# Optimization experiments

Hardware: AMD Instinct MI355X
Metric: run time of the kernel (lower is better)

## Reference

```python
import jax, jax.numpy as jnp
import numpy as np

INPUT_SIZE, HIDDEN, LEVELS = 64, 256, 2
T, B = 2048, 128


def _lstm_layer(x_seq, h0, c0, W_ih, W_hh, b_ih, b_hh):
    """Run one LSTM layer over the full sequence. x_seq: [T,B,D] -> hs: [T,B,H].
    PyTorch gate order: i, f, g, o."""
    def step(carry, x_t):
        h, c = carry
        z = x_t @ W_ih.T + b_ih + h @ W_hh.T + b_hh  # [B, 4H]
        i, f, g, o = jnp.split(z, 4, axis=-1)
        i = jax.nn.sigmoid(i)
        f = jax.nn.sigmoid(f)
        g = jnp.tanh(g)
        o = jax.nn.sigmoid(o)
        c = f * c + i * g
        h = o * jnp.tanh(c)
        return (h, c), h
    _, hs = jax.lax.scan(step, (h0, c0), x_seq)
    return hs


def setup_inputs() -> dict:
    key = jax.random.key(0)
    ks = jax.random.split(key, 16)
    s = 1.0 / np.sqrt(HIDDEN)
    inp = {
        "x": jax.random.normal(ks[0], (T, B, INPUT_SIZE), dtype=jnp.float32),
        "h0": jax.random.uniform(ks[1], (LEVELS, B, HIDDEN), dtype=jnp.float32),
        "c0": jax.random.uniform(ks[2], (LEVELS, B, HIDDEN), dtype=jnp.float32),
        # layer 0 (input -> hidden)
        "W_ih0": jax.random.uniform(ks[3], (4 * HIDDEN, INPUT_SIZE), jnp.float32, -s, s),
        "W_hh0": jax.random.uniform(ks[4], (4 * HIDDEN, HIDDEN), jnp.float32, -s, s),
        "b_ih0": jax.random.uniform(ks[5], (4 * HIDDEN,), jnp.float32, -s, s),
        "b_hh0": jax.random.uniform(ks[6], (4 * HIDDEN,), jnp.float32, -s, s),
        # layer 1 (hidden -> hidden)
        "W_ih1": jax.random.uniform(ks[7], (4 * HIDDEN, HIDDEN), jnp.float32, -s, s),
        "W_hh1": jax.random.uniform(ks[8], (4 * HIDDEN, HIDDEN), jnp.float32, -s, s),
        "b_ih1": jax.random.uniform(ks[9], (4 * HIDDEN,), jnp.float32, -s, s),
        "b_hh1": jax.random.uniform(ks[10], (4 * HIDDEN,), jnp.float32, -s, s),
        # linear head hidden -> 1
        "W_lin": jax.random.uniform(ks[11], (1, HIDDEN), jnp.float32, -s, s),
        "b_lin": jax.random.uniform(ks[12], (1,), jnp.float32, -s, s),
    }
    return inp


def reference(x, h0, c0, W_ih0, W_hh0, b_ih0, b_hh0, W_ih1, W_hh1, b_ih1, b_hh1, W_lin, b_lin):
    hs0 = _lstm_layer(x, h0[0], c0[0], W_ih0, W_hh0, b_ih0, b_hh0)   # [T,B,H]
    hs1 = _lstm_layer(hs0, h0[1], c0[1], W_ih1, W_hh1, b_ih1, b_hh1)  # [T,B,H]
    out = hs1 @ W_lin.T + b_lin  # [T,B,1]
    return out[..., 0]  # [T,B] (matches torch stack().squeeze())
```

## Files before the change

### kernel.cpp

```cpp
#include <hip/hip_runtime.h>

constexpr int TT   = 2048;
constexpr int NB   = 128;
constexpr int NI   = 64;
constexpr int NH   = 256;
constexpr int NGRP = 128;
constexpr int NWG  = 256;
constexpr int NTHR = 512;
constexpr int R0   = 8;
constexpr int R1   = 16;
constexpr int HLAG = 8;
constexpr int SLOT = (NH / 2) * NB;

__device__ __align__(256) unsigned g_p0[128];
__device__ __align__(256) unsigned g_p1[128];
__device__ unsigned g_cnt = 0, g_gen = 0;

__device__ __forceinline__ float sigm(float v) { return 1.0f / (1.0f + __expf(-v)); }
__device__ __forceinline__ float tanhfast(float v) {
    float e = __expf(2.0f * v);
    return 1.0f - 2.0f / (e + 1.0f);
}
__device__ __forceinline__ float asfl(unsigned u) { return __uint_as_float(u); }
__device__ __forceinline__ unsigned f2bf(float f) {
    unsigned u = __float_as_uint(f);
    return (u + 0x7fffu + ((u >> 16) & 1u)) >> 16;
}

__device__ __forceinline__ unsigned long long ldq(const unsigned* p) {
    return __hip_atomic_load((const unsigned long long*)p, __ATOMIC_RELAXED,
                             __HIP_MEMORY_SCOPE_AGENT);
}
__device__ __forceinline__ unsigned ldd(const unsigned* p) {
    return __hip_atomic_load(p, __ATOMIC_RELAXED, __HIP_MEMORY_SCOPE_AGENT);
}
__device__ __forceinline__ void std_(unsigned* p, unsigned v) {
    __hip_atomic_store(p, v, __ATOMIC_RELAXED, __HIP_MEMORY_SCOPE_AGENT);
}

__device__ __forceinline__ void pollall(unsigned n0, unsigned n1, int lane) {
    const unsigned* p0 = &g_p0[lane << 1];
    const unsigned* p1 = &g_p1[lane << 1];
    for (;;) {
        unsigned long long a = ldq(p0);
        unsigned long long b = ldq(p1);
        bool ok = ((unsigned)a >= n0) && ((unsigned)(a >> 32) >= n0) &&
                  ((unsigned)b >= n1) && ((unsigned)(b >> 32) >= n1);
        if (__all(ok)) return;
        __builtin_amdgcn_s_sleep(1);
    }
}

__device__ __forceinline__ void gridbar(unsigned k, bool last) {
    __syncthreads();
    if (threadIdx.x == 0) {
        __threadfence();
        unsigned a = __hip_atomic_fetch_add(&g_cnt, 1u, __ATOMIC_ACQ_REL,
                                            __HIP_MEMORY_SCOPE_AGENT);
        if (a == k * NWG - 1u) {
            if (last) {
                __hip_atomic_store(&g_cnt, 0u, __ATOMIC_RELAXED, __HIP_MEMORY_SCOPE_AGENT);
                __hip_atomic_store(&g_gen, 0u, __ATOMIC_RELEASE, __HIP_MEMORY_SCOPE_AGENT);
            } else {
                __hip_atomic_store(&g_gen, k, __ATOMIC_RELEASE, __HIP_MEMORY_SCOPE_AGENT);
            }
        } else if (!last) {
            while (__hip_atomic_load(&g_gen, __ATOMIC_RELAXED,
                                     __HIP_MEMORY_SCOPE_AGENT) < k)
                __builtin_amdgcn_s_sleep(1);
        }
        __threadfence();
    }
    __syncthreads();
}

#define STEPQ(Q, HA, HB)                                   \
    acc[0]  += w00.Q * (HA); acc[1]  += w00.Q * (HB);      \
    acc[2]  += w01.Q * (HA); acc[3]  += w01.Q * (HB);      \
    acc[4]  += w02.Q * (HA); acc[5]  += w02.Q * (HB);      \
    acc[6]  += w03.Q * (HA); acc[7]  += w03.Q * (HB);      \
    acc[8]  += w10.Q * (HA); acc[9]  += w10.Q * (HB);      \
    acc[10] += w11.Q * (HA); acc[11] += w11.Q * (HB);      \
    acc[12] += w12.Q * (HA); acc[13] += w12.Q * (HB);      \
    acc[14] += w13.Q * (HA); acc[15] += w13.Q * (HB);

#define LOADW(W, K, kk)                                                        \
    float4 w00 = *(const float4*)((W) + (size_t)(0 * NH + j0    ) * (K) + (kk)); \
    float4 w01 = *(const float4*)((W) + (size_t)(1 * NH + j0    ) * (K) + (kk)); \
    float4 w02 = *(const float4*)((W) + (size_t)(2 * NH + j0    ) * (K) + (kk)); \
    float4 w03 = *(const float4*)((W) + (size_t)(3 * NH + j0    ) * (K) + (kk)); \
    float4 w10 = *(const float4*)((W) + (size_t)(0 * NH + j0 + 1) * (K) + (kk)); \
    float4 w11 = *(const float4*)((W) + (size_t)(1 * NH + j0 + 1) * (K) + (kk)); \
    float4 w12 = *(const float4*)((W) + (size_t)(2 * NH + j0 + 1) * (K) + (kk)); \
    float4 w13 = *(const float4*)((W) + (size_t)(3 * NH + j0 + 1) * (K) + (kk));

__device__ __forceinline__ void partH_bf(const float* __restrict__ W, int j0,
                                         int kbase,
                                         const unsigned* __restrict__ hd,
                                         int lane, float* acc) {
    const unsigned* hp = hd + (size_t)(kbase >> 1) * NB + (lane << 1);
    #pragma unroll 4
    for (int i = 0; i < 16; ++i) {
        const int kk = kbase + (i << 2);
        LOADW(W, NH, kk)
        unsigned long long q0 = ldq(hp + (size_t)(2 * i) * NB);
        unsigned long long q1 = ldq(hp + (size_t)(2 * i + 1) * NB);
        unsigned d00 = (unsigned)q0, d01 = (unsigned)(q0 >> 32);
        unsigned d10 = (unsigned)q1, d11 = (unsigned)(q1 >> 32);
        STEPQ(x, asfl(d00 << 16),          asfl(d01 << 16))
        STEPQ(y, asfl(d00 & 0xffff0000u),  asfl(d01 & 0xffff0000u))
        STEPQ(z, asfl(d10 << 16),          asfl(d11 << 16))
        STEPQ(w, asfl(d10 & 0xffff0000u),  asfl(d11 & 0xffff0000u))
    }
}

__device__ __forceinline__ void partX(const float* __restrict__ W, int j0,
                                      int k0, const float* __restrict__ xp,
                                      int lane, float* acc) {
    #pragma unroll
    for (int i4 = 0; i4 < 4; ++i4) {
        const int kk = k0 + (i4 << 2);
        LOADW(W, NI, kk)
        float4 xa = *(const float4*)(xp + (size_t)(lane << 1) * NI + kk);
        float4 xb = *(const float4*)(xp + (size_t)((lane << 1) + 1) * NI + kk);
        STEPQ(x, xa.x, xb.x)
        STEPQ(y, xa.y, xb.y)
        STEPQ(z, xa.z, xb.z)
        STEPQ(w, xa.w, xb.w)
    }
}

__global__ void __launch_bounds__(NTHR, 2) lstm2(
    const float* __restrict__ x,
    const float* __restrict__ h0in, const float* __restrict__ c0in,
    const float* __restrict__ Wih0, const float* __restrict__ Whh0,
    const float* __restrict__ bih0, const float* __restrict__ bhh0,
    const float* __restrict__ Wih1, const float* __restrict__ Whh1,
    const float* __restrict__ bih1, const float* __restrict__ bhh1,
    const float* __restrict__ Wlin, const float* __restrict__ blin,
    float* __restrict__ out,
    unsigned* __restrict__ h0d, unsigned* __restrict__ h1d)
{
    __shared__ __align__(16) float4 zp4[16 * NB];
    __shared__ float red[4];
    __shared__ unsigned go_w;

    const int tid  = threadIdx.x;
    const int gid  = blockIdx.x;
    const bool is1 = gid >= NGRP;
    const int g    = is1 ? gid - NGRP : gid;
    const int j0   = g * 2;
    const int lane = tid & 63;
    const int wv   = __builtin_amdgcn_readfirstlane(tid >> 6);

    unsigned* ownp = is1 ? g_p1 : g_p0;

    float4 bsA = make_float4(0, 0, 0, 0), bsB = bsA;
    float cA = 0.f, cB = 0.f;
    if (tid < 128) {
        const float* bi = is1 ? bih1 : bih0;
        const float* bh = is1 ? bhh1 : bhh0;
        bsA.x = bi[0 * NH + j0] + bh[0 * NH + j0];
        bsA.y = bi[1 * NH + j0] + bh[1 * NH + j0];
        bsA.z = bi[2 * NH + j0] + bh[2 * NH + j0];
        bsA.w = bi[3 * NH + j0] + bh[3 * NH + j0];
        bsB.x = bi[0 * NH + j0 + 1] + bh[0 * NH + j0 + 1];
        bsB.y = bi[1 * NH + j0 + 1] + bh[1 * NH + j0 + 1];
        bsB.z = bi[2 * NH + j0 + 1] + bh[2 * NH + j0 + 1];
        bsB.w = bi[3 * NH + j0 + 1] + bh[3 * NH + j0 + 1];
        const float* cbase = c0in + (is1 ? 1 : 0) * NB * NH + (size_t)tid * NH + j0;
        cA = cbase[0]; cB = cbase[1];
        const float* hbase = h0in + (is1 ? 1 : 0) * NB * NH + (size_t)tid * NH + j0;
        unsigned d = (f2bf(hbase[1]) << 16) | f2bf(hbase[0]);
        unsigned* hT = is1 ? h1d : h0d;
        const int islot = is1 ? (R1 - 1) : (R0 - 1);
        std_(hT + (size_t)islot * SLOT + (size_t)g * NB + tid, d);
    }
    if (tid == 0) go_w = 0;
    const float blv = blin[0];
    asm volatile("s_waitcnt vmcnt(0)" ::: "memory");
    __syncthreads();
    if (tid == 0) std_(&ownp[g], 1u);

    if (!is1) {
        for (int s = 0; s < TT + HLAG; ++s) {
            const unsigned tgt = (unsigned)(s + 1);
            unsigned need0 = (s < TT) ? (unsigned)(s + 1) : 0u;
            unsigned need1 = (s >= R0) ? (unsigned)(s - R0 + 2) : 0u;
            if (wv == 0) {
                pollall(need0, need1, lane);
                if (lane == 0)
                    __hip_atomic_store(&go_w, tgt, __ATOMIC_RELAXED,
                                       __HIP_MEMORY_SCOPE_WORKGROUP);
            } else {
                while (__hip_atomic_load(&go_w, __ATOMIC_RELAXED,
                                         __HIP_MEMORY_SCOPE_WORKGROUP) < tgt) {}
            }

            if (s < TT) {
                float acc[16] = {0,0,0,0,0,0,0,0,0,0,0,0,0,0,0,0};
                if (wv < 4)
                    partH_bf(Whh0, j0, wv * 64,
                             h0d + (size_t)((s + R0 - 1) & (R0 - 1)) * SLOT, lane, acc);
                else
                    partX(Wih0, j0, (wv - 4) * 16, x + (size_t)s * NB * NI, lane, acc);
                const int base0 = ((wv << 1) + 0) * NB + (lane << 1);
                const int base1 = ((wv << 1) + 1) * NB + (lane << 1);
                zp4[base0]     = make_float4(acc[0],  acc[2],  acc[4],  acc[6]);
                zp4[base0 + 1] = make_float4(acc[1],  acc[3],  acc[5],  acc[7]);
                zp4[base1]     = make_float4(acc[8],  acc[10], acc[12], acc[14]);
                zp4[base1 + 1] = make_float4(acc[9],  acc[11], acc[13], acc[15]);
            }
            if (s >= HLAG && tid >= 256) {
                const int u = s - HLAG;
                const int k = tid - 256;
                unsigned d = ldd(h1d + (size_t)(u & (R1 - 1)) * SLOT
                                 + (size_t)(k >> 1) * NB + g);
                float hv = (k & 1) ? asfl(d & 0xffff0000u) : asfl(d << 16);
                float p = Wlin[k] * hv;
                #pragma unroll
                for (int off = 32; off; off >>= 1) p += __shfl_down(p, off);
                if (lane == 0) red[wv - 4] = p;
            }
            __syncthreads();

            if (s < TT && tid < 128) {
                float4 zA = bsA, zB = bsB;
                #pragma unroll
                for (int q = 0; q < 8; ++q) {
                    float4 a = zp4[(q * 2 + 0) * NB + tid];
                    float4 b = zp4[(q * 2 + 1) * NB + tid];
                    zA.x += a.x; zA.y += a.y; zA.z += a.z; zA.w += a.w;
                    zB.x += b.x; zB.y += b.y; zB.z += b.z; zB.w += b.w;
                }
                float iA = sigm(zA.x), fA = sigm(zA.y), gA = tanhfast(zA.z), oA = sigm(zA.w);
                cA = fA * cA + iA * gA;
                float hA = oA * tanhfast(cA);
                float iB = sigm(zB.x), fB = sigm(zB.y), gB = tanhfast(zB.z), oB = sigm(zB.w);
                cB = fB * cB + iB * gB;
                float hB = oB * tanhfast(cB);
                unsigned d = (f2bf(hB) << 16) | f2bf(hA);
                std_(h0d + (size_t)(s & (R0 - 1)) * SLOT + (size_t)g * NB + tid, d);
            }
            if (s >= HLAG && tid == 256)
                out[(size_t)(s - HLAG) * NB + g] = red[0] + red[1] + red[2] + red[3] + blv;

            asm volatile("s_waitcnt vmcnt(0)" ::: "memory");
            __syncthreads();
            if (s < TT && tid == 0) std_(&g_p0[g], (unsigned)(s + 2));
        }
    } else {
        for (int t = 0; t < TT; ++t) {
            const unsigned tgt = (unsigned)(t + 1);
            unsigned need0 = (unsigned)(t + 2);
            unsigned need1 = (unsigned)(t + 1);
            if (wv == 0) {
                pollall(need0, need1, lane);
                if (lane == 0)
                    __hip_atomic_store(&go_w, tgt, __ATOMIC_RELAXED,
                                       __HIP_MEMORY_SCOPE_WORKGROUP);
            } else {
                while (__hip_atomic_load(&go_w, __ATOMIC_RELAXED,
                                         __HIP_MEMORY_SCOPE_WORKGROUP) < tgt) {}
            }

            float acc[16] = {0,0,0,0,0,0,0,0,0,0,0,0,0,0,0,0};
            if (wv < 4)
                partH_bf(Wih1, j0, wv * 64,
                         h0d + (size_t)(t & (R0 - 1)) * SLOT, lane, acc);
            else
                partH_bf(Whh1, j0, (wv - 4) * 64,
                         h1d + (size_t)((t + R1 - 1) & (R1 - 1)) * SLOT, lane, acc);
            const int base0 = ((wv << 1) + 0) * NB + (lane << 1);
            const int base1 = ((wv << 1) + 1) * NB + (lane << 1);
            zp4[base0]     = make_float4(acc[0],  acc[2],  acc[4],  acc[6]);
            zp4[base0 + 1] = make_float4(acc[1],  acc[3],  acc[5],  acc[7]);
            zp4[base1]     = make_float4(acc[8],  acc[10], acc[12], acc[14]);
            zp4[base1 + 1] = make_float4(acc[9],  acc[11], acc[13], acc[15]);
            __syncthreads();

            if (tid < 128) {
                float4 zA = bsA, zB = bsB;
                #pragma unroll
                for (int q = 0; q < 8; ++q) {
                    float4 a = zp4[(q * 2 + 0) * NB + tid];
                    float4 b = zp4[(q * 2 + 1) * NB + tid];
                    zA.x += a.x; zA.y += a.y; zA.z += a.z; zA.w += a.w;
                    zB.x += b.x; zB.y += b.y; zB.z += b.z; zB.w += b.w;
                }
                float iA = sigm(zA.x), fA = sigm(zA.y), gA = tanhfast(zA.z), oA = sigm(zA.w);
                cA = fA * cA + iA * gA;
                float hA = oA * tanhfast(cA);
                float iB = sigm(zB.x), fB = sigm(zB.y), gB = tanhfast(zB.z), oB = sigm(zB.w);
                cB = fB * cB + iB * gB;
                float hB = oB * tanhfast(cB);
                unsigned d = (f2bf(hB) << 16) | f2bf(hA);
                std_(h1d + (size_t)(t & (R1 - 1)) * SLOT + (size_t)g * NB + tid, d);
            }
            asm volatile("s_waitcnt vmcnt(0)" ::: "memory");
            __syncthreads();
            if (tid == 0) std_(&g_p1[g], (unsigned)(t + 2));
        }
    }

    gridbar(1, false);
    if (gid == 0 && tid < 128) {
        std_(&g_p0[tid], 0u);
        std_(&g_p1[tid], 0u);
    }
    asm volatile("s_waitcnt vmcnt(0)" ::: "memory");
    gridbar(2, true);
}

extern "C" void kernel_launch(void* const* d_in, const int* in_sizes, int n_in,
                              void* d_out, int out_size, void* d_ws, size_t ws_size,
                              hipStream_t stream)
{
    const float* x    = (const float*)d_in[0];
    const float* h0in = (const float*)d_in[1];
    const float* c0in = (const float*)d_in[2];
    const float* Wih0 = (const float*)d_in[3];
    const float* Whh0 = (const float*)d_in[4];
    const float* bih0 = (const float*)d_in[5];
    const float* bhh0 = (const float*)d_in[6];
    const float* Wih1 = (const float*)d_in[7];
    const float* Whh1 = (const float*)d_in[8];
    const float* bih1 = (const float*)d_in[9];
    const float* bhh1 = (const float*)d_in[10];
    const float* Wlin = (const float*)d_in[11];
    const float* blin = (const float*)d_in[12];
    float* out = (float*)d_out;

    unsigned* h0d = (unsigned*)d_ws;
    unsigned* h1d = h0d + (size_t)R0 * SLOT;

    void* args[] = { &x, &h0in, &c0in, &Wih0, &Whh0, &bih0, &bhh0,
                     &Wih1, &Whh1, &bih1, &bhh1, &Wlin, &blin,
                     &out, &h0d, &h1d };
    hipLaunchCooperativeKernel((void*)lstm2, dim3(NWG), dim3(NTHR), args, 0, stream);
}
```

Before: 23.03 ms.

## Repartition LSTM work: four hidden units by half batch per workgroup

Each workgroup now owns 4 hidden units across 64 batch columns instead of 2 hidden units across all 128 columns. Each lane handles one batch column against two pairs of weight rows, instead of two columns against one pair. The shared-memory partial-sum layout, the gate reduction indexing and the bf16 h-state write addressing are rewritten to match. The aim is to halve the h-state each workgroup reads from global memory per step. In exchange, per-workgroup weight traffic doubles and each lane loads narrower h values.

```diff
diff --git a/kernel.cpp b/kernel.cpp
--- a/kernel.cpp
+++ b/kernel.cpp
@@ -74,59 +74,64 @@
     __syncthreads();
 }
 
-#define STEPQ(Q, HA, HB)                                   \
-    acc[0]  += w00.Q * (HA); acc[1]  += w00.Q * (HB);      \
-    acc[2]  += w01.Q * (HA); acc[3]  += w01.Q * (HB);      \
-    acc[4]  += w02.Q * (HA); acc[5]  += w02.Q * (HB);      \
-    acc[6]  += w03.Q * (HA); acc[7]  += w03.Q * (HB);      \
-    acc[8]  += w10.Q * (HA); acc[9]  += w10.Q * (HB);      \
-    acc[10] += w11.Q * (HA); acc[11] += w11.Q * (HB);      \
-    acc[12] += w12.Q * (HA); acc[13] += w12.Q * (HB);      \
-    acc[14] += w13.Q * (HA); acc[15] += w13.Q * (HB);
-
-#define LOADW(W, K, kk)                                                        \
-    float4 w00 = *(const float4*)((W) + (size_t)(0 * NH + j0    ) * (K) + (kk)); \
-    float4 w01 = *(const float4*)((W) + (size_t)(1 * NH + j0    ) * (K) + (kk)); \
-    float4 w02 = *(const float4*)((W) + (size_t)(2 * NH + j0    ) * (K) + (kk)); \
-    float4 w03 = *(const float4*)((W) + (size_t)(3 * NH + j0    ) * (K) + (kk)); \
-    float4 w10 = *(const float4*)((W) + (size_t)(0 * NH + j0 + 1) * (K) + (kk)); \
-    float4 w11 = *(const float4*)((W) + (size_t)(1 * NH + j0 + 1) * (K) + (kk)); \
-    float4 w12 = *(const float4*)((W) + (size_t)(2 * NH + j0 + 1) * (K) + (kk)); \
-    float4 w13 = *(const float4*)((W) + (size_t)(3 * NH + j0 + 1) * (K) + (kk));
-
-__device__ __forceinline__ void partH_bf(const float* __restrict__ W, int j0,
-                                         int kbase,
-                                         const unsigned* __restrict__ hd,
-                                         int lane, float* acc) {
-    const unsigned* hp = hd + (size_t)(kbase >> 1) * NB + (lane << 1);
+#define LOADWJ(W, K, kk, jj)                                                       \
+    float4 w00 = *(const float4*)((W) + (size_t)(0 * NH + (jj)    ) * (K) + (kk)); \
+    float4 w01 = *(const float4*)((W) + (size_t)(1 * NH + (jj)    ) * (K) + (kk)); \
+    float4 w02 = *(const float4*)((W) + (size_t)(2 * NH + (jj)    ) * (K) + (kk)); \
+    float4 w03 = *(const float4*)((W) + (size_t)(3 * NH + (jj)    ) * (K) + (kk)); \
+    float4 w10 = *(const float4*)((W) + (size_t)(0 * NH + (jj) + 1) * (K) + (kk)); \
+    float4 w11 = *(const float4*)((W) + (size_t)(1 * NH + (jj) + 1) * (K) + (kk)); \
+    float4 w12 = *(const float4*)((W) + (size_t)(2 * NH + (jj) + 1) * (K) + (kk)); \
+    float4 w13 = *(const float4*)((W) + (size_t)(3 * NH + (jj) + 1) * (K) + (kk));
+
+#define STEP1(Q, H, A)                                     \
+    (A)[0] += w00.Q * (H); (A)[1] += w01.Q * (H);          \
+    (A)[2] += w02.Q * (H); (A)[3] += w03.Q * (H);          \
+    (A)[4] += w10.Q * (H); (A)[5] += w11.Q * (H);          \
+    (A)[6] += w12.Q * (H); (A)[7] += w13.Q * (H);
+
+__device__ __forceinline__ void partH4(const float* __restrict__ W, int j0,
+                                       int kbase,
+                                       const unsigned* __restrict__ hd,
+                                       int col, float* acc) {
+    const unsigned* hp = hd + (size_t)(kbase >> 1) * NB + col;
     #pragma unroll 4
     for (int i = 0; i < 16; ++i) {
         const int kk = kbase + (i << 2);
-        LOADW(W, NH, kk)
-        unsigned long long q0 = ldq(hp + (size_t)(2 * i) * NB);
-        unsigned long long q1 = ldq(hp + (size_t)(2 * i + 1) * NB);
-        unsigned d00 = (unsigned)q0, d01 = (unsigned)(q0 >> 32);
-        unsigned d10 = (unsigned)q1, d11 = (unsigned)(q1 >> 32);
-        STEPQ(x, asfl(d00 << 16),          asfl(d01 << 16))
-        STEPQ(y, asfl(d00 & 0xffff0000u),  asfl(d01 & 0xffff0000u))
-        STEPQ(z, asfl(d10 << 16),          asfl(d11 << 16))
-        STEPQ(w, asfl(d10 & 0xffff0000u),  asfl(d11 & 0xffff0000u))
-    }
-}
-
-__device__ __forceinline__ void partX(const float* __restrict__ W, int j0,
-                                      int k0, const float* __restrict__ xp,
-                                      int lane, float* acc) {
+        unsigned d0 = ldd(hp + (size_t)(2 * i) * NB);
+        unsigned d1 = ldd(hp + (size_t)(2 * i + 1) * NB);
+        float hx = asfl(d0 << 16), hy = asfl(d0 & 0xffff0000u);
+        float hz = asfl(d1 << 16), hw = asfl(d1 & 0xffff0000u);
+        {
+            LOADWJ(W, NH, kk, j0)
+            STEP1(x, hx, acc) STEP1(y, hy, acc)
+            STEP1(z, hz, acc) STEP1(w, hw, acc)
+        }
+        {
+            LOADWJ(W, NH, kk, j0 + 2)
+            STEP1(x, hx, acc + 8) STEP1(y, hy, acc + 8)
+            STEP1(z, hz, acc + 8) STEP1(w, hw, acc + 8)
+        }
+    }
+}
+
+__device__ __forceinline__ void partX4(const float* __restrict__ W, int j0,
+                                       int k0, const float* __restrict__ xp,
+                                       float* acc) {
     #pragma unroll
     for (int i4 = 0; i4 < 4; ++i4) {
         const int kk = k0 + (i4 << 2);
-        LOADW(W, NI, kk)
-        float4 xa = *(const float4*)(xp + (size_t)(lane << 1) * NI + kk);
-        float4 xb = *(const float4*)(xp + (size_t)((lane << 1) + 1) * NI + kk);
-        STEPQ(x, xa.x, xb.x)
-        STEPQ(y, xa.y, xb.y)
-        STEPQ(z, xa.z, xb.z)
-        STEPQ(w, xa.w, xb.w)
+        float4 xv = *(const float4*)(xp + kk);
+        {
+            LOADWJ(W, NI, kk, j0)
+            STEP1(x, xv.x, acc) STEP1(y, xv.y, acc)
+            STEP1(z, xv.z, acc) STEP1(w, xv.w, acc)
+        }
+        {
+            LOADWJ(W, NI, kk, j0 + 2)
+            STEP1(x, xv.x, acc + 8) STEP1(y, xv.y, acc + 8)
+            STEP1(z, xv.z, acc + 8) STEP1(w, xv.w, acc + 8)
+        }
     }
 }
 
@@ -141,7 +146,7 @@
     float* __restrict__ out,
     unsigned* __restrict__ h0d, unsigned* __restrict__ h1d)
 {
-    __shared__ __align__(16) float4 zp4[16 * NB];
+    __shared__ __align__(16) float4 zp4[32 * 64];
     __shared__ float red[4];
     __shared__ unsigned go_w;
 
@@ -149,7 +154,9 @@
     const int gid  = blockIdx.x;
     const bool is1 = gid >= NGRP;
     const int g    = is1 ? gid - NGRP : gid;
-    const int j0   = g * 2;
+    const int jg   = g & 63;
+    const int j0   = jg * 4;
+    const int b0   = (g >> 6) * 64;
     const int lane = tid & 63;
     const int wv   = __builtin_amdgcn_readfirstlane(tid >> 6);
 
@@ -158,23 +165,26 @@
     float4 bsA = make_float4(0, 0, 0, 0), bsB = bsA;
     float cA = 0.f, cB = 0.f;
     if (tid < 128) {
+        const int bcol = b0 + (tid >> 1);
+        const int jp   = tid & 1;
+        const int jc   = j0 + 2 * jp;
         const float* bi = is1 ? bih1 : bih0;
         const float* bh = is1 ? bhh1 : bhh0;
-        bsA.x = bi[0 * NH + j0] + bh[0 * NH + j0];
-        bsA.y = bi[1 * NH + j0] + bh[1 * NH + j0];
-        bsA.z = bi[2 * NH + j0] + bh[2 * NH + j0];
-        bsA.w = bi[3 * NH + j0] + bh[3 * NH + j0];
-        bsB.x = bi[0 * NH + j0 + 1] + bh[0 * NH + j0 + 1];
-        bsB.y = bi[1 * NH + j0 + 1] + bh[1 * NH + j0 + 1];
-        bsB.z = bi[2 * NH + j0 + 1] + bh[2 * NH + j0 + 1];
-        bsB.w = bi[3 * NH + j0 + 1] + bh[3 * NH + j0 + 1];
-        const float* cbase = c0in + (is1 ? 1 : 0) * NB * NH + (size_t)tid * NH + j0;
+        bsA.x = bi[0 * NH + jc] + bh[0 * NH + jc];
+        bsA.y = bi[1 * NH + jc] + bh[1 * NH + jc];
+        bsA.z = bi[2 * NH + jc] + bh[2 * NH + jc];
+        bsA.w = bi[3 * NH + jc] + bh[3 * NH + jc];
+        bsB.x = bi[0 * NH + jc + 1] + bh[0 * NH + jc + 1];
+        bsB.y = bi[1 * NH + jc + 1] + bh[1 * NH + jc + 1];
+        bsB.z = bi[2 * NH + jc + 1] + bh[2 * NH + jc + 1];
+        bsB.w = bi[3 * NH + jc + 1] + bh[3 * NH + jc + 1];
+        const float* cbase = c0in + (is1 ? 1 : 0) * NB * NH + (size_t)bcol * NH + jc;
         cA = cbase[0]; cB = cbase[1];
-        const float* hbase = h0in + (is1 ? 1 : 0) * NB * NH + (size_t)tid * NH + j0;
+        const float* hbase = h0in + (is1 ? 1 : 0) * NB * NH + (size_t)bcol * NH + jc;
         unsigned d = (f2bf(hbase[1]) << 16) | f2bf(hbase[0]);
         unsigned* hT = is1 ? h1d : h0d;
         const int islot = is1 ? (R1 - 1) : (R0 - 1);
-        std_(hT + (size_t)islot * SLOT + (size_t)g * NB + tid, d);
+        std_(hT + (size_t)islot * SLOT + (size_t)((j0 >> 1) + jp) * NB + bcol, d);
     }
     if (tid == 0) go_w = 0;
     const float blv = blin[0];
@@ -200,16 +210,17 @@
             if (s < TT) {
                 float acc[16] = {0,0,0,0,0,0,0,0,0,0,0,0,0,0,0,0};
                 if (wv < 4)
-                    partH_bf(Whh0, j0, wv * 64,
-                             h0d + (size_t)((s + R0 - 1) & (R0 - 1)) * SLOT, lane, acc);
+                    partH4(Whh0, j0, wv * 64,
+                           h0d + (size_t)((s + R0 - 1) & (R0 - 1)) * SLOT,
+                           b0 + lane, acc);
                 else
-                    partX(Wih0, j0, (wv - 4) * 16, x + (size_t)s * NB * NI, lane, acc);
-                const int base0 = ((wv << 1) + 0) * NB + (lane << 1);
-                const int base1 = ((wv << 1) + 1) * NB + (lane << 1);
-                zp4[base0]     = make_float4(acc[0],  acc[2],  acc[4],  acc[6]);
-                zp4[base0 + 1] = make_float4(acc[1],  acc[3],  acc[5],  acc[7]);
-                zp4[base1]     = make_float4(acc[8],  acc[10], acc[12], acc[14]);
-                zp4[base1 + 1] = make_float4(acc[9],  acc[11], acc[13], acc[15]);
+                    partX4(Wih0, j0, (wv - 4) * 16,
+                           x + (size_t)s * NB * NI + (size_t)(b0 + lane) * NI, acc);
+                const int zb = (wv << 2) * 64 + lane;
+                zp4[zb]       = make_float4(acc[0],  acc[1],  acc[2],  acc[3]);
+                zp4[zb + 64]  = make_float4(acc[4],  acc[5],  acc[6],  acc[7]);
+                zp4[zb + 128] = make_float4(acc[8],  acc[9],  acc[10], acc[11]);
+                zp4[zb + 192] = make_float4(acc[12], acc[13], acc[14], acc[15]);
             }
             if (s >= HLAG && tid >= 256) {
                 const int u = s - HLAG;
@@ -225,11 +236,12 @@
             __syncthreads();
 
             if (s < TT && tid < 128) {
+                const int bl = tid >> 1, jp = tid & 1;
                 float4 zA = bsA, zB = bsB;
                 #pragma unroll
                 for (int q = 0; q < 8; ++q) {
-                    float4 a = zp4[(q * 2 + 0) * NB + tid];
-                    float4 b = zp4[(q * 2 + 1) * NB + tid];
+                    float4 a = zp4[((q << 2) + 2 * jp) * 64 + bl];
+                    float4 b = zp4[((q << 2) + 2 * jp + 1) * 64 + bl];
                     zA.x += a.x; zA.y += a.y; zA.z += a.z; zA.w += a.w;
                     zB.x += b.x; zB.y += b.y; zB.z += b.z; zB.w += b.w;
                 }
@@ -240,7 +252,8 @@
                 cB = fB * cB + iB * gB;
                 float hB = oB * tanhfast(cB);
                 unsigned d = (f2bf(hB) << 16) | f2bf(hA);
-                std_(h0d + (size_t)(s & (R0 - 1)) * SLOT + (size_t)g * NB + tid, d);
+                std_(h0d + (size_t)(s & (R0 - 1)) * SLOT
+                     + (size_t)((j0 >> 1) + jp) * NB + (b0 + bl), d);
             }
             if (s >= HLAG && tid == 256)
                 out[(size_t)(s - HLAG) * NB + g] = red[0] + red[1] + red[2] + red[3] + blv;
@@ -266,25 +279,25 @@
 
             float acc[16] = {0,0,0,0,0,0,0,0,0,0,0,0,0,0,0,0};
             if (wv < 4)
-                partH_bf(Wih1, j0, wv * 64,
-                         h0d + (size_t)(t & (R0 - 1)) * SLOT, lane, acc);
+                partH4(Wih1, j0, wv * 64,
+                       h0d + (size_t)(t & (R0 - 1)) * SLOT, b0 + lane, acc);
             else
-                partH_bf(Whh1, j0, (wv - 4) * 64,
-                         h1d + (size_t)((t + R1 - 1) & (R1 - 1)) * SLOT, lane, acc);
-            const int base0 = ((wv << 1) + 0) * NB + (lane << 1);
-            const int base1 = ((wv << 1) + 1) * NB + (lane << 1);
-            zp4[base0]     = make_float4(acc[0],  acc[2],  acc[4],  acc[6]);
-            zp4[base0 + 1] = make_float4(acc[1],  acc[3],  acc[5],  acc[7]);
-            zp4[base1]     = make_float4(acc[8],  acc[10], acc[12], acc[14]);
-            zp4[base1 + 1] = make_float4(acc[9],  acc[11], acc[13], acc[15]);
+                partH4(Whh1, j0, (wv - 4) * 64,
+                       h1d + (size_t)((t + R1 - 1) & (R1 - 1)) * SLOT, b0 + lane, acc);
+            const int zb = (wv << 2) * 64 + lane;
+            zp4[zb]       = make_float4(acc[0],  acc[1],  acc[2],  acc[3]);
+            zp4[zb + 64]  = make_float4(acc[4],  acc[5],  acc[6],  acc[7]);
+            zp4[zb + 128] = make_float4(acc[8],  acc[9],  acc[10], acc[11]);
+            zp4[zb + 192] = make_float4(acc[12], acc[13], acc[14], acc[15]);
             __syncthreads();
 
             if (tid < 128) {
+                const int bl = tid >> 1, jp = tid & 1;
                 float4 zA = bsA, zB = bsB;
                 #pragma unroll
                 for (int q = 0; q < 8; ++q) {
-                    float4 a = zp4[(q * 2 + 0) * NB + tid];
-                    float4 b = zp4[(q * 2 + 1) * NB + tid];
+                    float4 a = zp4[((q << 2) + 2 * jp) * 64 + bl];
+                    float4 b = zp4[((q << 2) + 2 * jp + 1) * 64 + bl];
                     zA.x += a.x; zA.y += a.y; zA.z += a.z; zA.w += a.w;
                     zB.x += b.x; zB.y += b.y; zB.z += b.z; zB.w += b.w;
                 }
@@ -295,7 +308,8 @@
                 cB = fB * cB + iB * gB;
                 float hB = oB * tanhfast(cB);
                 unsigned d = (f2bf(hB) << 16) | f2bf(hA);
-                std_(h1d + (size_t)(t & (R1 - 1)) * SLOT + (size_t)g * NB + tid, d);
+                std_(h1d + (size_t)(t & (R1 - 1)) * SLOT
+                     + (size_t)((j0 >> 1) + jp) * NB + (b0 + bl), d);
             }
             asm volatile("s_waitcnt vmcnt(0)" ::: "memory");
             __syncthreads();
```

Measured after the change: 39.00 ms. +69.3%, slower.

## Replace per-block wave-0 polling with per-wave dependency-specific flag polling

Applied to the files above, without the earlier changes.

Each wave now polls only the progress flags of the producer blocks whose hidden-state slice it actually reads, instead of wave 0 polling all 256 flags and releasing the others through a shared-memory go flag. This is meant to cut the polling latency and the LDS handoff on the critical per-timestep path, and lets waves start as soon as their own inputs are ready. In exchange more waves issue global atomic loads each step, which raises L2 traffic. Correctness now depends on each wave's 32-flag subset matching exactly the h columns it consumes.

```diff
diff --git a/kernel.cpp b/kernel.cpp
--- a/kernel.cpp
+++ b/kernel.cpp
@@ -38,15 +38,20 @@
     __hip_atomic_store(p, v, __ATOMIC_RELAXED, __HIP_MEMORY_SCOPE_AGENT);
 }
 
-__device__ __forceinline__ void pollall(unsigned n0, unsigned n1, int lane) {
-    const unsigned* p0 = &g_p0[lane << 1];
-    const unsigned* p1 = &g_p1[lane << 1];
+__device__ __forceinline__ void pollsub(const unsigned* p, unsigned n) {
+    const int l = threadIdx.x & 31;
     for (;;) {
-        unsigned long long a = ldq(p0);
-        unsigned long long b = ldq(p1);
-        bool ok = ((unsigned)a >= n0) && ((unsigned)(a >> 32) >= n0) &&
-                  ((unsigned)b >= n1) && ((unsigned)(b >> 32) >= n1);
-        if (__all(ok)) return;
+        unsigned v = ldd(p + l);
+        if (__all(v >= n)) return;
+        __builtin_amdgcn_s_sleep(1);
+    }
+}
+
+__device__ __forceinline__ void poll128(const unsigned* arr, unsigned n) {
+    const unsigned* p = arr + ((threadIdx.x & 63) << 1);
+    for (;;) {
+        unsigned long long a = ldq(p);
+        if (__all(((unsigned)a >= n) && ((unsigned)(a >> 32) >= n))) return;
         __builtin_amdgcn_s_sleep(1);
     }
 }
@@ -143,7 +148,6 @@
 {
     __shared__ __align__(16) float4 zp4[16 * NB];
     __shared__ float red[4];
-    __shared__ unsigned go_w;
 
     const int tid  = threadIdx.x;
     const int gid  = blockIdx.x;
@@ -176,7 +180,6 @@
         const int islot = is1 ? (R1 - 1) : (R0 - 1);
         std_(hT + (size_t)islot * SLOT + (size_t)g * NB + tid, d);
     }
-    if (tid == 0) go_w = 0;
     const float blv = blin[0];
     asm volatile("s_waitcnt vmcnt(0)" ::: "memory");
     __syncthreads();
@@ -184,18 +187,10 @@
 
     if (!is1) {
         for (int s = 0; s < TT + HLAG; ++s) {
-            const unsigned tgt = (unsigned)(s + 1);
-            unsigned need0 = (s < TT) ? (unsigned)(s + 1) : 0u;
-            unsigned need1 = (s >= R0) ? (unsigned)(s - R0 + 2) : 0u;
-            if (wv == 0) {
-                pollall(need0, need1, lane);
-                if (lane == 0)
-                    __hip_atomic_store(&go_w, tgt, __ATOMIC_RELAXED,
-                                       __HIP_MEMORY_SCOPE_WORKGROUP);
-            } else {
-                while (__hip_atomic_load(&go_w, __ATOMIC_RELAXED,
-                                         __HIP_MEMORY_SCOPE_WORKGROUP) < tgt) {}
-            }
+            if (s < TT && wv < 4)
+                pollsub(&g_p0[wv * 32], (unsigned)(s + 1));
+            if (wv >= 4 && s >= R0)
+                poll128(g_p1, (unsigned)(s - R0 + 2));
 
             if (s < TT) {
                 float acc[16] = {0,0,0,0,0,0,0,0,0,0,0,0,0,0,0,0};
@@ -251,18 +246,10 @@
         }
     } else {
         for (int t = 0; t < TT; ++t) {
-            const unsigned tgt = (unsigned)(t + 1);
-            unsigned need0 = (unsigned)(t + 2);
-            unsigned need1 = (unsigned)(t + 1);
-            if (wv == 0) {
-                pollall(need0, need1, lane);
-                if (lane == 0)
-                    __hip_atomic_store(&go_w, tgt, __ATOMIC_RELAXED,
-                                       __HIP_MEMORY_SCOPE_WORKGROUP);
-            } else {
-                while (__hip_atomic_load(&go_w, __ATOMIC_RELAXED,
-                                         __HIP_MEMORY_SCOPE_WORKGROUP) < tgt) {}
-            }
+            if (wv < 4)
+                pollsub(&g_p0[wv * 32], (unsigned)(t + 2));
+            else
+                pollsub(&g_p1[(wv - 4) * 32], (unsigned)(t + 1));
 
             float acc[16] = {0,0,0,0,0,0,0,0,0,0,0,0,0,0,0,0};
             if (wv < 4)
```

New measurement: 26.91 ms. +16.9%, slower.
